# Kernel tuning notes

Hardware: AMD Instinct MI355X
Metric: run time of the kernel (lower is better)

The kernel has to match this reference:

```python
import jax, jax.numpy as jnp
import numpy as np

DIM = 512
HEADS = 8
HEAD_DIM = DIM // HEADS
R = 2  # reduce_ratio
SCALE = HEAD_DIM ** -0.5


def setup_inputs() -> dict:
    key = jax.random.key(0)
    ks = jax.random.split(key, 8)
    bs, H, W = 4, 64, 64
    n = H * W
    std = 0.02
    x = jax.random.normal(ks[0], (bs, n, DIM), dtype=jnp.float32)
    q_w = jax.random.normal(ks[1], (DIM, DIM), dtype=jnp.float32) * std
    kv_w = jax.random.normal(ks[2], (DIM, 2 * DIM), dtype=jnp.float32) * std
    proj_w = jax.random.normal(ks[3], (DIM, DIM), dtype=jnp.float32) * std
    proj_b = jnp.zeros((DIM,), dtype=jnp.float32)
    # Conv2d(dim, dim, kernel=R, stride=R), kaiming-like init
    fan_out = R * R * DIM
    sr_w = jax.random.normal(ks[4], (DIM, DIM, R, R), dtype=jnp.float32) * np.sqrt(2.0 / fan_out)
    sr_b = jnp.zeros((DIM,), dtype=jnp.float32)
    ln_w = jnp.ones((DIM,), dtype=jnp.float32)
    ln_b = jnp.zeros((DIM,), dtype=jnp.float32)
    return {"x": x, "q_w": q_w, "kv_w": kv_w, "proj_w": proj_w, "proj_b": proj_b,
            "sr_w": sr_w, "sr_b": sr_b, "ln_w": ln_w, "ln_b": ln_b, "H": H, "W": W}


def _layernorm(x, w, b, eps=1e-5):
    mu = jnp.mean(x, axis=-1, keepdims=True)
    var = jnp.var(x, axis=-1, keepdims=True)
    return (x - mu) * jax.lax.rsqrt(var + eps) * w + b


def reference(x, q_w, kv_w, proj_w, proj_b, sr_w, sr_b, ln_w, ln_b, H, W):
    bs, n, ch = x.shape
    # q: (bs, heads, n, head_dim)
    q = (x @ q_w).reshape(bs, n, HEADS, HEAD_DIM).transpose(0, 2, 1, 3)
    # spatial reduction of kv source: strided conv + layernorm
    x_img = x.transpose(0, 2, 1).reshape(bs, ch, H, W)
    xr = jax.lax.conv_general_dilated(
        x_img, sr_w, window_strides=(R, R), padding='VALID',
        dimension_numbers=('NCHW', 'OIHW', 'NCHW')) + sr_b[None, :, None, None]
    xr = xr.reshape(bs, ch, -1).transpose(0, 2, 1)  # (bs, n_kv, ch)
    xr = _layernorm(xr, ln_w, ln_b)
    kv = xr @ kv_w  # (bs, n_kv, 2*ch)
    n_kv = kv.shape[1]
    kv = kv.reshape(bs, n_kv, 2, HEADS, HEAD_DIM).transpose(2, 0, 3, 1, 4)
    k, v = kv[0], kv[1]  # (bs, heads, n_kv, head_dim)
    att = jnp.einsum('bhqd,bhkd->bhqk', q, k) * SCALE
    att = jax.nn.softmax(att, axis=-1)
    net = jnp.einsum('bhqk,bhkd->bhqd', att, v)
    net = net.transpose(0, 2, 1, 3).reshape(bs, n, ch)
    return net @ proj_w + proj_b
```

## Files before the change

### kernel.cpp

```cpp
#include <hip/hip_runtime.h>
#include <cstdint>

#define HEADS 8
#define HD 64
#define NQ 4096
#define NKV 1024

typedef unsigned short u16;
typedef __attribute__((ext_vector_type(8))) short short8;
typedef __attribute__((ext_vector_type(4))) float f32x4;
typedef __attribute__((ext_vector_type(16))) float f32x16;

__device__ __forceinline__ u16 f2bf(float f){
  union { float f; unsigned u; } c; c.f = f;
  unsigned r = c.u + 0x7fffu + ((c.u >> 16) & 1u);
  return (u16)(r >> 16);
}
__device__ __forceinline__ unsigned pack2(float a, float b){
  return (unsigned)f2bf(a) | ((unsigned)f2bf(b) << 16);
}
__device__ __forceinline__ float fexp2(float x){
  float r;
  asm("v_exp_f32 %0, %1" : "=v"(r) : "v"(x));
  return r;
}
__device__ __forceinline__ unsigned cvtpk(float a, float b){
  unsigned r;
  asm("v_cvt_pk_bf16_f32 %0, %1, %2" : "=v"(r) : "v"(a), "v"(b));
  return r;
}
__device__ __forceinline__ void gll16(const void* g, void* l){
  __builtin_amdgcn_global_load_lds((const __attribute__((address_space(1))) unsigned*)g,
                                   (__attribute__((address_space(3))) unsigned*)l, 16, 0, 0);
}
#define SB0() __builtin_amdgcn_sched_barrier(0)
#define MFMA16(a, b, c) __builtin_amdgcn_mfma_f32_16x16x32_bf16(a, b, c, 0, 0, 0)
#define MFMA32(a, b, c) __builtin_amdgcn_mfma_f32_32x32x16_bf16(a, b, c, 0, 0, 0)
#define Z16 {0.f,0.f,0.f,0.f,0.f,0.f,0.f,0.f,0.f,0.f,0.f,0.f,0.f,0.f,0.f,0.f}

__global__ __launch_bounds__(256) void prep_x(const float* __restrict__ x,
                                              u16* __restrict__ x_bf,
                                              u16* __restrict__ a_conv){
  int tid = blockIdx.x * 256 + threadIdx.x;
  int b   = tid >> 18;
  int rem = tid & 262143;
  int pos = rem >> 6;
  int ci0 = (rem & 63) << 3;
  size_t src = ((size_t)(b * NQ + pos)) * 512 + ci0;
  const float4* s4 = (const float4*)(x + src);
  float4 v0 = s4[0], v1 = s4[1];
  uint4 p;
  p.x = pack2(v0.x, v0.y); p.y = pack2(v0.z, v0.w);
  p.z = pack2(v1.x, v1.y); p.w = pack2(v1.z, v1.w);
  *(uint4*)(x_bf + src) = p;
  int h = pos >> 6, w = pos & 63;
  int pr = (h >> 1) * 32 + (w >> 1);
  int t  = (h & 1) * 2 + (w & 1);
  *(uint4*)(a_conv + ((size_t)(b * NKV + pr)) * 2048 + t * 512 + ci0) = p;
}

__global__ __launch_bounds__(256) void prep_w(const float* __restrict__ q_w,
                                              const float* __restrict__ kv_w,
                                              const float* __restrict__ proj_w,
                                              const float* __restrict__ sr_w,
                                              u16* __restrict__ q_wT, u16* __restrict__ kv_wT,
                                              u16* __restrict__ proj_wT, u16* __restrict__ conv_BT){
  int e = blockIdx.x * 256 + threadIdx.x;
  if (e < 262144){ int n = e >> 9, k = e & 511; q_wT[e] = f2bf(q_w[k * 512 + n]); return; }
  e -= 262144;
  if (e < 524288){ int n = e >> 9, k = e & 511; kv_wT[e] = f2bf(kv_w[k * 1024 + n]); return; }
  e -= 524288;
  if (e < 262144){ int n = e >> 9, k = e & 511; proj_wT[e] = f2bf(proj_w[k * 512 + n]); return; }
  e -= 262144;
  { int co = e >> 11, r = e & 2047, t = r >> 9, ci = r & 511;
    conv_BT[e] = f2bf(sr_w[co * 2048 + ci * 4 + t]); }
}

template<int MODE>
__global__ __launch_bounds__(256) void gemm_bt(const u16* __restrict__ A, const u16* __restrict__ BT,
                                               float* __restrict__ Cf, float* __restrict__ Cf2,
                                               u16* __restrict__ Cb0,
                                               u16* __restrict__ Cb1, const float* __restrict__ bias,
                                               int M, int N, int K){
  __shared__ __align__(16) u16 As[128 * 64];
  __shared__ __align__(16) u16 Bs[128 * 64];
  const int tid = threadIdx.x, lane = tid & 63, wave = tid >> 6;
  const int l15 = lane & 15, g = lane >> 4, r7 = l15 & 7;
  const int m0 = blockIdx.y * 128, n0 = blockIdx.x * 128;
  const int wr = wave >> 1, wc = wave & 1;
  const int kz = blockIdx.z;
  const int klen = K / (int)gridDim.z;
  const int kb = kz * klen;
  f32x4 acc[4][4] = {};
  for (int kt = kb; kt < kb + klen; kt += 64){
    #pragma unroll
    for (int i = 0; i < 4; ++i){
      int c = i * 256 + tid;
      int row = c >> 3, sc = (c & 7) ^ (row & 7);
      gll16(A  + (size_t)(m0 + row) * K + kt + sc * 8, As + (size_t)(i * 256 + wave * 64) * 8);
      gll16(BT + (size_t)(n0 + row) * K + kt + sc * 8, Bs + (size_t)(i * 256 + wave * 64) * 8);
    }
    __syncthreads();
    #pragma unroll
    for (int kk = 0; kk < 2; ++kk){
      short8 af[4];
      #pragma unroll
      for (int mi = 0; mi < 4; ++mi)
        af[mi] = *(const short8*)(As + (wr * 64 + mi * 16 + l15) * 64 + (((kk * 4 + g) ^ r7) << 3));
      #pragma unroll
      for (int ni = 0; ni < 4; ++ni){
        short8 bf = *(const short8*)(Bs + (wc * 64 + ni * 16 + l15) * 64 + (((kk * 4 + g) ^ r7) << 3));
        #pragma unroll
        for (int mi = 0; mi < 4; ++mi)
          acc[mi][ni] = MFMA16(af[mi], bf, acc[mi][ni]);
      }
    }
    __syncthreads();
  }
  #pragma unroll
  for (int mi = 0; mi < 4; ++mi){
    int row = m0 + wr * 64 + mi * 16 + (lane >> 4) * 4;
    #pragma unroll
    for (int ni = 0; ni < 4; ++ni){
      int col = n0 + wc * 64 + ni * 16 + l15;
      f32x4 v = acc[mi][ni];
      if (MODE == 0){
        float* Co = (kz < 2) ? (Cf + (size_t)kz * M * N) : (Cf2 + (size_t)(kz - 2) * M * N);
        float bb = (bias && kz == 0) ? bias[col] : 0.f;
        #pragma unroll
        for (int j = 0; j < 4; ++j) Co[(size_t)(row + j) * N + col] = v[j] + bb;
      } else if (MODE == 1){
        int h = col >> 6, d = col & 63;
        #pragma unroll
        for (int j = 0; j < 4; ++j){
          int r = row + j, b = r >> 12, nq = r & 4095;
          Cb0[(((size_t)(b * HEADS + h)) * NQ + nq) * HD + d] = f2bf(v[j] * 0.18033688f);
        }
      } else {
        int s = col >> 9, h = (col >> 6) & 7, d = col & 63;
        if (s == 0){
          #pragma unroll
          for (int j = 0; j < 4; ++j){
            int r = row + j, b = r >> 10, p = r & 1023;
            Cb0[(((size_t)(b * HEADS + h)) * NKV + p) * HD + d] = f2bf(v[j]);
          }
        } else {
          int b = row >> 10, p0 = row & 1023;
          int pp = (p0 & ~12) | (((p0 >> 2) & 1) << 3) | (((p0 >> 3) & 1) << 2);
          ushort4 pk;
          pk.x = f2bf(v[0]); pk.y = f2bf(v[1]); pk.z = f2bf(v[2]); pk.w = f2bf(v[3]);
          *(ushort4*)(Cb1 + (((size_t)(b * HEADS + h)) * HD + d) * NKV + pp) = pk;
        }
      }
    }
  }
}

__global__ __launch_bounds__(256) void ln_k(const float* __restrict__ xp, const float* __restrict__ xp2,
                                            const float* __restrict__ w,
                                            const float* __restrict__ bias, u16* __restrict__ xr){
  int row = blockIdx.x * 4 + (threadIdx.x >> 6);
  int lane = threadIdx.x & 63;
  const float* s1 = xp  + (size_t)row * 512;
  const float* s2 = s1 + (size_t)4096 * 512;
  const float* s3 = xp2 + (size_t)row * 512;
  const float* s4 = s3 + (size_t)4096 * 512;
  float vals[8]; float s = 0.f, ss = 0.f;
  #pragma unroll
  for (int j = 0; j < 8; ++j){
    int c = lane + j * 64;
    float v = (s1[c] + s2[c]) + (s3[c] + s4[c]);
    vals[j] = v; s += v; ss += v * v;
  }
  #pragma unroll
  for (int off = 32; off >= 1; off >>= 1){ s += __shfl_xor(s, off); ss += __shfl_xor(ss, off); }
  float mean = s * (1.f / 512.f);
  float var  = ss * (1.f / 512.f) - mean * mean;
  float rs = rsqrtf(var + 1e-5f);
  u16* dst = xr + (size_t)row * 512;
  #pragma unroll
  for (int j = 0; j < 8; ++j){
    int c = lane + j * 64;
    dst[c] = f2bf((vals[j] - mean) * rs * w[c] + bias[c]);
  }
}

template<bool LAST>
__device__ __forceinline__ void attn_tile(const u16* ksb, const u16* vsb,
                                          u16* kstage, u16* vstage,
                                          const u16* akg, const u16* avg,
                                          const short8* qf,
                                          int l31, int hi, int x7,
                                          f32x16* o, float& l_run){
  SB0();
  if (!LAST){
    gll16(akg,              kstage);
    gll16(akg + 2048,       kstage + 2048);
    gll16(avg,              vstage);
    gll16(avg + 32 * 1024,  vstage + 2048);
    SB0();
    asm volatile("s_waitcnt vmcnt(4)" ::: "memory");
  } else {
    asm volatile("s_waitcnt vmcnt(0)" ::: "memory");
  }
  __builtin_amdgcn_s_barrier();
  SB0();

  f32x16 sa[2];
  __builtin_amdgcn_s_setprio(1);
  #pragma unroll
  for (int sub = 0; sub < 2; ++sub){
    f32x16 a = Z16;
    #pragma unroll
    for (int ks = 0; ks < 4; ++ks){
      short8 kf = *(const short8*)(ksb + (sub * 32 + l31) * 64 + (((ks * 2 + hi) ^ x7) << 3));
      a = MFMA32(kf, qf[ks], a);
    }
    sa[sub] = a;
  }
  __builtin_amdgcn_s_setprio(0);

  unsigned w[16];
  float ps = 0.f;
  #pragma unroll
  for (int sub = 0; sub < 2; ++sub)
    #pragma unroll
    for (int t = 0; t < 8; ++t){
      float p0 = fexp2(sa[sub][2 * t]), p1 = fexp2(sa[sub][2 * t + 1]);
      ps += p0 + p1;
      w[sub * 8 + t] = cvtpk(p0, p1);
    }
  l_run += ps;

  __builtin_amdgcn_s_setprio(1);
  #pragma unroll
  for (int dt = 0; dt < 2; ++dt)
    #pragma unroll
    for (int sl = 0; sl < 4; ++sl){
      short8 vf = *(const short8*)(vsb + (dt * 32 + l31) * 64 + (((sl * 2 + hi) ^ x7) << 3));
      union { unsigned u[4]; short8 s; } bb;
      bb.u[0] = w[sl * 4 + 0]; bb.u[1] = w[sl * 4 + 1];
      bb.u[2] = w[sl * 4 + 2]; bb.u[3] = w[sl * 4 + 3];
      o[dt] = MFMA32(vf, bb.s, o[dt]);
    }
  __builtin_amdgcn_s_setprio(0);
  SB0();
  __builtin_amdgcn_s_barrier();
}

__global__ __launch_bounds__(256) void attn_k(const u16* __restrict__ q_s, const u16* __restrict__ k_s,
                                              const u16* __restrict__ vt_s, u16* __restrict__ net){
  __shared__ __align__(16) u16 Ks[2][64 * 64];
  __shared__ __align__(16) u16 Vt[2][64 * 64];
  const int tid = threadIdx.x, lane = tid & 63, wave = tid >> 6;
  const int l31 = lane & 31, hi = lane >> 5, x7 = lane & 7;
  const int bh = blockIdx.y;
  const u16* kb  = k_s  + (size_t)bh * NKV * HD;
  const u16* vtb = vt_s + (size_t)bh * HD * NKV;
  const int q0 = blockIdx.x * 128 + wave * 32;
  const u16* qbase = q_s + ((size_t)bh * NQ + q0 + l31) * HD + hi * 8;
  short8 qf[4];
  #pragma unroll
  for (int ks = 0; ks < 4; ++ks) qf[ks] = *(const short8*)(qbase + ks * 16);

  const int swz8 = (((tid & 7) ^ ((tid >> 3) & 7)) << 3);
  const u16* ak0 = kb  + (size_t)(tid >> 3) * 64   + swz8;
  const u16* av0 = vtb + (size_t)(tid >> 3) * 1024 + swz8;

  f32x16 o[2] = { Z16, Z16 };
  float l_run = 0.f;

  gll16(ak0,             &Ks[0][wave * 512]);
  gll16(ak0 + 2048,      &Ks[0][2048 + wave * 512]);
  gll16(av0,             &Vt[0][wave * 512]);
  gll16(av0 + 32 * 1024, &Vt[0][2048 + wave * 512]);

  for (int tt = 0; tt < 7; ++tt){
    attn_tile<false>(&Ks[0][0], &Vt[0][0], &Ks[1][wave * 512], &Vt[1][wave * 512],
                     ak0 + (size_t)(2 * tt + 1) * 4096, av0 + (2 * tt + 1) * 64,
                     qf, l31, hi, x7, o, l_run);
    attn_tile<false>(&Ks[1][0], &Vt[1][0], &Ks[0][wave * 512], &Vt[0][wave * 512],
                     ak0 + (size_t)(2 * tt + 2) * 4096, av0 + (2 * tt + 2) * 64,
                     qf, l31, hi, x7, o, l_run);
  }
  attn_tile<false>(&Ks[0][0], &Vt[0][0], &Ks[1][wave * 512], &Vt[1][wave * 512],
                   ak0 + (size_t)15 * 4096, av0 + 15 * 64,
                   qf, l31, hi, x7, o, l_run);
  attn_tile<true>(&Ks[1][0], &Vt[1][0], nullptr, nullptr, nullptr, nullptr,
                  qf, l31, hi, x7, o, l_run);

  float l = l_run + __shfl_xor(l_run, 32);
  float inv = 1.f / l;
  int b = bh >> 3, h = bh & 7;
  size_t obase = ((size_t)b * NQ + q0 + l31) * 512 + h * 64;
  #pragma unroll
  for (int dt = 0; dt < 2; ++dt)
    #pragma unroll
    for (int t = 0; t < 8; ++t){
      int j = 2 * t;
      int d = dt * 32 + (j & 3) + 8 * (j >> 2) + 4 * hi;
      *(unsigned*)(net + obase + d) = cvtpk(o[dt][j] * inv, o[dt][j + 1] * inv);
    }
}

extern "C" void kernel_launch(void* const* d_in, const int* in_sizes, int n_in,
                              void* d_out, int out_size, void* d_ws, size_t ws_size,
                              hipStream_t stream){
  const float* x      = (const float*)d_in[0];
  const float* q_w    = (const float*)d_in[1];
  const float* kv_w   = (const float*)d_in[2];
  const float* proj_w = (const float*)d_in[3];
  const float* proj_b = (const float*)d_in[4];
  const float* sr_w   = (const float*)d_in[5];
  const float* sr_b   = (const float*)d_in[6];
  const float* ln_w   = (const float*)d_in[7];
  const float* ln_b   = (const float*)d_in[8];
  (void)in_sizes; (void)n_in; (void)out_size; (void)ws_size;

  char* ws = (char*)d_ws;
  u16*   x_bf    = (u16*)(ws);
  float* xr_pre2 = (float*)(ws);
  u16*   a_conv  = (u16*)(ws + ((size_t)16 << 20));
  u16*   xr      = (u16*)(ws + ((size_t)16 << 20));
  u16*   net     = (u16*)(ws + ((size_t)16 << 20));
  u16*   q_sb    = (u16*)(ws + ((size_t)32 << 20));
  float* xr_pre  = (float*)(ws + ((size_t)48 << 20));
  u16*   k_sb    = (u16*)(ws + ((size_t)48 << 20));
  u16*   vt_sb   = (u16*)(ws + ((size_t)52 << 20));
  u16*   q_wT    = (u16*)(ws + ((size_t)64 << 20));
  u16*   kv_wT   = (u16*)(ws + ((size_t)64 << 20) + 524288);
  u16*   proj_wT = (u16*)(ws + ((size_t)64 << 20) + 524288 + 1048576);
  u16*   conv_BT = (u16*)(ws + ((size_t)64 << 20) + 524288 + 1048576 + 524288);
  float* out = (float*)d_out;

  prep_w<<<8192, 256, 0, stream>>>(q_w, kv_w, proj_w, sr_w, q_wT, kv_wT, proj_wT, conv_BT);
  prep_x<<<4096, 256, 0, stream>>>(x, x_bf, a_conv);
  gemm_bt<1><<<dim3(4, 128), 256, 0, stream>>>(x_bf, q_wT, nullptr, nullptr, q_sb, nullptr, nullptr, 16384, 512, 512);
  gemm_bt<0><<<dim3(4, 32, 4), 256, 0, stream>>>(a_conv, conv_BT, xr_pre, xr_pre2, nullptr, nullptr, sr_b, 4096, 512, 2048);
  ln_k<<<1024, 256, 0, stream>>>(xr_pre, xr_pre2, ln_w, ln_b, xr);
  gemm_bt<2><<<dim3(8, 32),  256, 0, stream>>>(xr, kv_wT, nullptr, nullptr, k_sb, vt_sb, nullptr, 4096, 1024, 512);
  attn_k<<<dim3(32, 32), 256, 0, stream>>>(q_sb, k_sb, vt_sb, net);
  gemm_bt<0><<<dim3(4, 128), 256, 0, stream>>>(net, proj_wT, out, nullptr, nullptr, nullptr, proj_b, 16384, 512, 512);
}
```

Measured before the change: 147.5 us.

## Double per-wave query rows in attention, remap blocks to XCDs, merge prep kernels

After: 156.5 us. 6.1% more time.

```diff
diff --git a/kernel.cpp b/kernel.cpp
--- a/kernel.cpp
+++ b/kernel.cpp
@@ -38,34 +38,36 @@
 #define MFMA32(a, b, c) __builtin_amdgcn_mfma_f32_32x32x16_bf16(a, b, c, 0, 0, 0)
 #define Z16 {0.f,0.f,0.f,0.f,0.f,0.f,0.f,0.f,0.f,0.f,0.f,0.f,0.f,0.f,0.f,0.f}
 
-__global__ __launch_bounds__(256) void prep_x(const float* __restrict__ x,
-                                              u16* __restrict__ x_bf,
-                                              u16* __restrict__ a_conv){
-  int tid = blockIdx.x * 256 + threadIdx.x;
-  int b   = tid >> 18;
-  int rem = tid & 262143;
-  int pos = rem >> 6;
-  int ci0 = (rem & 63) << 3;
-  size_t src = ((size_t)(b * NQ + pos)) * 512 + ci0;
-  const float4* s4 = (const float4*)(x + src);
-  float4 v0 = s4[0], v1 = s4[1];
-  uint4 p;
-  p.x = pack2(v0.x, v0.y); p.y = pack2(v0.z, v0.w);
-  p.z = pack2(v1.x, v1.y); p.w = pack2(v1.z, v1.w);
-  *(uint4*)(x_bf + src) = p;
-  int h = pos >> 6, w = pos & 63;
-  int pr = (h >> 1) * 32 + (w >> 1);
-  int t  = (h & 1) * 2 + (w & 1);
-  *(uint4*)(a_conv + ((size_t)(b * NKV + pr)) * 2048 + t * 512 + ci0) = p;
-}
-
-__global__ __launch_bounds__(256) void prep_w(const float* __restrict__ q_w,
-                                              const float* __restrict__ kv_w,
-                                              const float* __restrict__ proj_w,
-                                              const float* __restrict__ sr_w,
-                                              u16* __restrict__ q_wT, u16* __restrict__ kv_wT,
-                                              u16* __restrict__ proj_wT, u16* __restrict__ conv_BT){
-  int e = blockIdx.x * 256 + threadIdx.x;
+__global__ __launch_bounds__(256) void prep_all(const float* __restrict__ x,
+                                                const float* __restrict__ q_w,
+                                                const float* __restrict__ kv_w,
+                                                const float* __restrict__ proj_w,
+                                                const float* __restrict__ sr_w,
+                                                u16* __restrict__ x_bf,
+                                                u16* __restrict__ a_conv,
+                                                u16* __restrict__ q_wT, u16* __restrict__ kv_wT,
+                                                u16* __restrict__ proj_wT, u16* __restrict__ conv_BT){
+  int bid = blockIdx.x;
+  if (bid < 4096){
+    int tid = bid * 256 + threadIdx.x;
+    int b   = tid >> 18;
+    int rem = tid & 262143;
+    int pos = rem >> 6;
+    int ci0 = (rem & 63) << 3;
+    size_t src = ((size_t)(b * NQ + pos)) * 512 + ci0;
+    const float4* s4 = (const float4*)(x + src);
+    float4 v0 = s4[0], v1 = s4[1];
+    uint4 p;
+    p.x = pack2(v0.x, v0.y); p.y = pack2(v0.z, v0.w);
+    p.z = pack2(v1.x, v1.y); p.w = pack2(v1.z, v1.w);
+    *(uint4*)(x_bf + src) = p;
+    int h = pos >> 6, w = pos & 63;
+    int pr = (h >> 1) * 32 + (w >> 1);
+    int t  = (h & 1) * 2 + (w & 1);
+    *(uint4*)(a_conv + ((size_t)(b * NKV + pr)) * 2048 + t * 512 + ci0) = p;
+    return;
+  }
+  int e = (bid - 4096) * 256 + threadIdx.x;
   if (e < 262144){ int n = e >> 9, k = e & 511; q_wT[e] = f2bf(q_w[k * 512 + n]); return; }
   e -= 262144;
   if (e < 524288){ int n = e >> 9, k = e & 511; kv_wT[e] = f2bf(kv_w[k * 1024 + n]); return; }
@@ -189,9 +191,10 @@
 __device__ __forceinline__ void attn_tile(const u16* ksb, const u16* vsb,
                                           u16* kstage, u16* vstage,
                                           const u16* akg, const u16* avg,
-                                          const short8* qf,
+                                          const short8* qfA, const short8* qfB,
                                           int l31, int hi, int x7,
-                                          f32x16* o, float& l_run){
+                                          f32x16* oA, f32x16* oB,
+                                          float& lA, float& lB){
   SB0();
   if (!LAST){
     gll16(akg,              kstage);
@@ -206,31 +209,30 @@
   __builtin_amdgcn_s_barrier();
   SB0();
 
-  f32x16 sa[2];
-  __builtin_amdgcn_s_setprio(1);
+  unsigned wA[16], wB[16];
+  float psA = 0.f, psB = 0.f;
   #pragma unroll
   for (int sub = 0; sub < 2; ++sub){
-    f32x16 a = Z16;
+    f32x16 aA = Z16, aB = Z16;
+    __builtin_amdgcn_s_setprio(1);
     #pragma unroll
     for (int ks = 0; ks < 4; ++ks){
       short8 kf = *(const short8*)(ksb + (sub * 32 + l31) * 64 + (((ks * 2 + hi) ^ x7) << 3));
-      a = MFMA32(kf, qf[ks], a);
-    }
-    sa[sub] = a;
-  }
-  __builtin_amdgcn_s_setprio(0);
-
-  unsigned w[16];
-  float ps = 0.f;
-  #pragma unroll
-  for (int sub = 0; sub < 2; ++sub)
+      aA = MFMA32(kf, qfA[ks], aA);
+      aB = MFMA32(kf, qfB[ks], aB);
+    }
+    __builtin_amdgcn_s_setprio(0);
     #pragma unroll
     for (int t = 0; t < 8; ++t){
-      float p0 = fexp2(sa[sub][2 * t]), p1 = fexp2(sa[sub][2 * t + 1]);
-      ps += p0 + p1;
-      w[sub * 8 + t] = cvtpk(p0, p1);
-    }
-  l_run += ps;
+      float a0 = fexp2(aA[2 * t]), a1 = fexp2(aA[2 * t + 1]);
+      psA += a0 + a1;
+      wA[sub * 8 + t] = cvtpk(a0, a1);
+      float b0 = fexp2(aB[2 * t]), b1 = fexp2(aB[2 * t + 1]);
+      psB += b0 + b1;
+      wB[sub * 8 + t] = cvtpk(b0, b1);
+    }
+  }
+  lA += psA; lB += psB;
 
   __builtin_amdgcn_s_setprio(1);
   #pragma unroll
@@ -238,10 +240,13 @@
     #pragma unroll
     for (int sl = 0; sl < 4; ++sl){
       short8 vf = *(const short8*)(vsb + (dt * 32 + l31) * 64 + (((sl * 2 + hi) ^ x7) << 3));
-      union { unsigned u[4]; short8 s; } bb;
-      bb.u[0] = w[sl * 4 + 0]; bb.u[1] = w[sl * 4 + 1];
-      bb.u[2] = w[sl * 4 + 2]; bb.u[3] = w[sl * 4 + 3];
-      o[dt] = MFMA32(vf, bb.s, o[dt]);
+      union { unsigned u[4]; short8 s; } bA, bB;
+      bA.u[0] = wA[sl * 4 + 0]; bA.u[1] = wA[sl * 4 + 1];
+      bA.u[2] = wA[sl * 4 + 2]; bA.u[3] = wA[sl * 4 + 3];
+      bB.u[0] = wB[sl * 4 + 0]; bB.u[1] = wB[sl * 4 + 1];
+      bB.u[2] = wB[sl * 4 + 2]; bB.u[3] = wB[sl * 4 + 3];
+      oA[dt] = MFMA32(vf, bA.s, oA[dt]);
+      oB[dt] = MFMA32(vf, bB.s, oB[dt]);
     }
   __builtin_amdgcn_s_setprio(0);
   SB0();
@@ -254,21 +259,27 @@
   __shared__ __align__(16) u16 Vt[2][64 * 64];
   const int tid = threadIdx.x, lane = tid & 63, wave = tid >> 6;
   const int l31 = lane & 31, hi = lane >> 5, x7 = lane & 7;
-  const int bh = blockIdx.y;
+  const int id = blockIdx.x;
+  const int xcd = id & 7, slot = id >> 3;
+  const int bh = 4 * xcd + (slot >> 4);
+  const int qblk = slot & 15;
   const u16* kb  = k_s  + (size_t)bh * NKV * HD;
   const u16* vtb = vt_s + (size_t)bh * HD * NKV;
-  const int q0 = blockIdx.x * 128 + wave * 32;
+  const int q0 = qblk * 256 + wave * 64;
   const u16* qbase = q_s + ((size_t)bh * NQ + q0 + l31) * HD + hi * 8;
-  short8 qf[4];
-  #pragma unroll
-  for (int ks = 0; ks < 4; ++ks) qf[ks] = *(const short8*)(qbase + ks * 16);
+  short8 qfA[4], qfB[4];
+  #pragma unroll
+  for (int ks = 0; ks < 4; ++ks){
+    qfA[ks] = *(const short8*)(qbase + ks * 16);
+    qfB[ks] = *(const short8*)(qbase + 32 * HD + ks * 16);
+  }
 
   const int swz8 = (((tid & 7) ^ ((tid >> 3) & 7)) << 3);
   const u16* ak0 = kb  + (size_t)(tid >> 3) * 64   + swz8;
   const u16* av0 = vtb + (size_t)(tid >> 3) * 1024 + swz8;
 
-  f32x16 o[2] = { Z16, Z16 };
-  float l_run = 0.f;
+  f32x16 oA[2] = { Z16, Z16 }, oB[2] = { Z16, Z16 };
+  float lA = 0.f, lB = 0.f;
 
   gll16(ak0,             &Ks[0][wave * 512]);
   gll16(ak0 + 2048,      &Ks[0][2048 + wave * 512]);
@@ -278,28 +289,31 @@
   for (int tt = 0; tt < 7; ++tt){
     attn_tile<false>(&Ks[0][0], &Vt[0][0], &Ks[1][wave * 512], &Vt[1][wave * 512],
                      ak0 + (size_t)(2 * tt + 1) * 4096, av0 + (2 * tt + 1) * 64,
-                     qf, l31, hi, x7, o, l_run);
+                     qfA, qfB, l31, hi, x7, oA, oB, lA, lB);
     attn_tile<false>(&Ks[1][0], &Vt[1][0], &Ks[0][wave * 512], &Vt[0][wave * 512],
                      ak0 + (size_t)(2 * tt + 2) * 4096, av0 + (2 * tt + 2) * 64,
-                     qf, l31, hi, x7, o, l_run);
+                     qfA, qfB, l31, hi, x7, oA, oB, lA, lB);
   }
   attn_tile<false>(&Ks[0][0], &Vt[0][0], &Ks[1][wave * 512], &Vt[1][wave * 512],
                    ak0 + (size_t)15 * 4096, av0 + 15 * 64,
-                   qf, l31, hi, x7, o, l_run);
+                   qfA, qfB, l31, hi, x7, oA, oB, lA, lB);
   attn_tile<true>(&Ks[1][0], &Vt[1][0], nullptr, nullptr, nullptr, nullptr,
-                  qf, l31, hi, x7, o, l_run);
-
-  float l = l_run + __shfl_xor(l_run, 32);
-  float inv = 1.f / l;
+                  qfA, qfB, l31, hi, x7, oA, oB, lA, lB);
+
+  float ltA = lA + __shfl_xor(lA, 32);
+  float ltB = lB + __shfl_xor(lB, 32);
+  float invA = 1.f / ltA, invB = 1.f / ltB;
   int b = bh >> 3, h = bh & 7;
-  size_t obase = ((size_t)b * NQ + q0 + l31) * 512 + h * 64;
+  size_t obaseA = ((size_t)b * NQ + q0 + l31) * 512 + h * 64;
+  size_t obaseB = obaseA + (size_t)32 * 512;
   #pragma unroll
   for (int dt = 0; dt < 2; ++dt)
     #pragma unroll
     for (int t = 0; t < 8; ++t){
       int j = 2 * t;
       int d = dt * 32 + (j & 3) + 8 * (j >> 2) + 4 * hi;
-      *(unsigned*)(net + obase + d) = cvtpk(o[dt][j] * inv, o[dt][j + 1] * inv);
+      *(unsigned*)(net + obaseA + d) = cvtpk(oA[dt][j] * invA, oA[dt][j + 1] * invA);
+      *(unsigned*)(net + obaseB + d) = cvtpk(oB[dt][j] * invB, oB[dt][j + 1] * invB);
     }
 }
 
@@ -333,12 +347,12 @@
   u16*   conv_BT = (u16*)(ws + ((size_t)64 << 20) + 524288 + 1048576 + 524288);
   float* out = (float*)d_out;
 
-  prep_w<<<8192, 256, 0, stream>>>(q_w, kv_w, proj_w, sr_w, q_wT, kv_wT, proj_wT, conv_BT);
-  prep_x<<<4096, 256, 0, stream>>>(x, x_bf, a_conv);
+  prep_all<<<12288, 256, 0, stream>>>(x, q_w, kv_w, proj_w, sr_w,
+                                      x_bf, a_conv, q_wT, kv_wT, proj_wT, conv_BT);
   gemm_bt<1><<<dim3(4, 128), 256, 0, stream>>>(x_bf, q_wT, nullptr, nullptr, q_sb, nullptr, nullptr, 16384, 512, 512);
   gemm_bt<0><<<dim3(4, 32, 4), 256, 0, stream>>>(a_conv, conv_BT, xr_pre, xr_pre2, nullptr, nullptr, sr_b, 4096, 512, 2048);
   ln_k<<<1024, 256, 0, stream>>>(xr_pre, xr_pre2, ln_w, ln_b, xr);
   gemm_bt<2><<<dim3(8, 32),  256, 0, stream>>>(xr, kv_wT, nullptr, nullptr, k_sb, vt_sb, nullptr, 4096, 1024, 512);
-  attn_k<<<dim3(32, 32), 256, 0, stream>>>(q_sb, k_sb, vt_sb, net);
+  attn_k<<<512, 256, 0, stream>>>(q_sb, k_sb, vt_sb, net);
   gemm_bt<0><<<dim3(4, 128), 256, 0, stream>>>(net, proj_wT, out, nullptr, nullptr, nullptr, proj_b, 16384, 512, 512);
 }
```
